# Kernel tuning notes

Measured on AMD Instinct MI355X. Metric: run time of the kernel, lower is better.

The kernel has to match this reference:

```python
import jax, jax.numpy as jnp
import numpy as np


def setup_inputs() -> dict:
    key = jax.random.key(0)
    ks = jax.random.split(key, 5)
    B, C, D, H, W = 2, 256, 8, 28, 28
    mid = C // 2
    # Kaiming-normal-ish init (std = sqrt(2/fan_in)) for 1x1 conv weights
    def kaiming(k, shape, fan_in):
        return jax.random.normal(k, shape, dtype=jnp.float32) * np.sqrt(2.0 / fan_in)
    x = jax.random.normal(ks[0], (B, C, D, H, W), dtype=jnp.float32)
    w1 = kaiming(ks[1], (mid, C), C)
    w2 = kaiming(ks[2], (mid, C), C)
    w3 = kaiming(ks[3], (mid, C), C)
    w4 = kaiming(ks[4], (C, mid), mid)
    b1 = jnp.zeros((mid,), jnp.float32)
    b2 = jnp.zeros((mid,), jnp.float32)
    b3 = jnp.zeros((mid,), jnp.float32)
    b4 = jnp.zeros((C,), jnp.float32)
    return {"x": x, "w1": w1, "b1": b1, "w2": w2, "b2": b2,
            "w3": w3, "b3": b3, "w4": w4, "b4": b4}


def reference(x, w1, b1, w2, b2, w3, b3, w4, b4):
    # x: [B, C, D, H, W]; 1x1x1 Conv3d == channel matmul over flattened N = D*H*W
    B, C, D, H, W = x.shape
    N = D * H * W
    xf = x.reshape(B, C, N)                                   # [B, C, N]
    # theta: conv1 -> [B, N, mid]
    e1 = jnp.einsum('mc,bcn->bnm', w1, xf) + b1               # [B, N, mid]
    # phi: conv2 -> [B, mid, N]
    e2 = jnp.einsum('mc,bcn->bmn', w2, xf) + b2[:, None]      # [B, mid, N]
    # g: conv3 -> [B, N, mid]
    e3 = jnp.einsum('mc,bcn->bnm', w3, xf) + b3               # [B, N, mid]
    # unscaled attention: softmax over keys (last axis)
    kernel = jnp.einsum('bnm,bmk->bnk', e1, e2)               # [B, N, N]
    kernel = jax.nn.softmax(kernel, axis=2)
    attn = jnp.einsum('bnk,bkm->bnm', kernel, e3)             # [B, N, mid]
    # conv4 (1x1 Conv1d): mid -> C, applied on [B, mid, N]
    y = jnp.einsum('cm,bnm->bcn', w4, attn) + b4[:, None]     # [B, C, N]
    return x + y.reshape(B, C, D, H, W)
```

## Files before the change

### kernel.cpp

```cpp
#include <hip/hip_runtime.h>


#define BB  2
#define CC  256
#define NN  6272
#define MID 128
#define KS  4
#define QB  128
#define NT  (NN / 64)
#define LOG2E 1.4426950408889634f

typedef _Float16 half2_t __attribute__((ext_vector_type(2)));
typedef _Float16 half4_t __attribute__((ext_vector_type(4)));
typedef _Float16 half8_t __attribute__((ext_vector_type(8)));
typedef float    floatx16 __attribute__((ext_vector_type(16)));
typedef int      i32x2 __attribute__((ext_vector_type(2)));
typedef unsigned u32x4 __attribute__((ext_vector_type(4)));

__device__ __forceinline__ void fma4(float4& a, const float4 v, const float s) {
    a.x += v.x * s; a.y += v.y * s; a.z += v.z * s; a.w += v.w * s;
}
__device__ __forceinline__ float dot4(const float4 a, const float4 b) {
    return a.x * b.x + a.y * b.y + a.z * b.z + a.w * b.w;
}
__device__ __forceinline__ unsigned pkrtz(float a, float b) {
    return __builtin_bit_cast(unsigned, __builtin_amdgcn_cvt_pkrtz(a, b));
}

__global__ __launch_bounds__(256, 2) void proj_kernel(
    const float* __restrict__ x,
    const float* __restrict__ w1, const float* __restrict__ bi1,
    const float* __restrict__ w2, const float* __restrict__ bi2,
    const float* __restrict__ w3, const float* __restrict__ bi3,
    _Float16* __restrict__ Qg, _Float16* __restrict__ Kg, _Float16* __restrict__ VtG)
{
    const int t  = threadIdx.x;
    const int n0 = blockIdx.x * 64;
    const int pj = blockIdx.y;
    const int b  = blockIdx.z;
    const float* w  = (pj == 0) ? w1 : (pj == 1) ? w2 : w3;
    const float* bi = (pj == 0) ? bi1 : (pj == 1) ? bi2 : bi3;
    const float qs  = (pj == 0) ? LOG2E : 1.0f;

    __shared__ float xs[CC * 68];
    {
        const float* xb = x + (size_t)b * CC * NN;
        for (int r = t; r < CC * 16; r += 256) {
            int c = r >> 4, j = (r & 15) << 2;
            float4 v = *(const float4*)(xb + (size_t)c * NN + n0 + j);
            *(float4*)&xs[c * 68 + j] = v;
        }
    }
    __syncthreads();

    const int n4 = (t & 15) << 2;
    const int m0 = (t >> 4) << 3;
    float4 acc4[8];
    #pragma unroll
    for (int k = 0; k < 8; ++k) acc4[k] = make_float4(0.f, 0.f, 0.f, 0.f);

    for (int cc = 0; cc < CC; cc += 4) {
        float4 xv[4];
        #pragma unroll
        for (int u = 0; u < 4; ++u)
            xv[u] = *(const float4*)&xs[(cc + u) * 68 + n4];
        #pragma unroll
        for (int k = 0; k < 8; ++k) {
            float4 wq = *(const float4*)(w + (size_t)(m0 + k) * CC + cc);
            fma4(acc4[k], xv[0], wq.x);
            fma4(acc4[k], xv[1], wq.y);
            fma4(acc4[k], xv[2], wq.z);
            fma4(acc4[k], xv[3], wq.w);
        }
    }

    const float* af = (const float*)acc4;
    float bb[8];
    #pragma unroll
    for (int k = 0; k < 8; ++k) bb[k] = bi[m0 + k];

    if (pj < 2) {
        _Float16* eo = ((pj == 0) ? Qg : Kg) + (size_t)b * NN * MID;
        #pragma unroll
        for (int i = 0; i < 4; ++i) {
            half8_t h;
            #pragma unroll
            for (int k = 0; k < 8; ++k) h[k] = (_Float16)((af[k * 4 + i] + bb[k]) * qs);
            *(half8_t*)(eo + (size_t)(n0 + n4 + i) * MID + m0) = h;
        }
    } else {
        _Float16* eo = VtG + (size_t)b * MID * NN;
        #pragma unroll
        for (int k = 0; k < 8; ++k) {
            half4_t h;
            #pragma unroll
            for (int i = 0; i < 4; ++i) h[i] = (_Float16)(af[k * 4 + i] + bb[k]);
            *(half4_t*)(eo + (size_t)(m0 + k) * NN + n0 + n4) = h;
        }
    }
}

__global__ __launch_bounds__(256, 2) void attn_kernel(
    const _Float16* __restrict__ Qg, const _Float16* __restrict__ Kg,
    const _Float16* __restrict__ VtG, _Float16* __restrict__ Opart,
    float* __restrict__ MLg)
{
    const int t    = threadIdx.x;
    const int lane = t & 63;
    const int wave = t >> 6;
    const int l31  = lane & 31;
    const int l5   = lane >> 5;
    const int q0   = blockIdx.x * QB;
    const int sp   = blockIdx.y;
    const int b    = blockIdx.z;
    const int kt0  = (NT * sp) / KS;
    const int kt1  = (NT * (sp + 1)) / KS;

    __shared__ __align__(16) char lds[52224];
    _Float16* Ks0 = (_Float16*)lds;
    _Float16* Ks1 = (_Float16*)(lds + 17408);
    _Float16* Vt  = (_Float16*)(lds + 34816);
    _Float16* Osh = (_Float16*)lds;

    const _Float16* Qb = Qg + ((size_t)b * NN + q0 + wave * 32) * MID;
    const _Float16* Kb = Kg + (size_t)b * NN * MID;
    const _Float16* Vb = VtG + (size_t)b * MID * NN;

    half8_t qf[8];
    #pragma unroll
    for (int ds = 0; ds < 8; ++ds)
        qf[ds] = *(const half8_t*)(Qb + (size_t)l31 * MID + ds * 16 + l5 * 8);

    floatx16 o[4];
    #pragma unroll
    for (int dt = 0; dt < 4; ++dt)
        #pragma unroll
        for (int j = 0; j < 16; ++j) o[dt][j] = 0.f;
    float m_run = -3.0e38f, l_run = 0.f;

    const int krow_t = t >> 4, koff_t = (t & 15) * 8;
    const int vd_t   = t >> 3, voff_t = (t & 7) * 8;

    #pragma unroll
    for (int it = 0; it < 4; ++it) {
        int r = it * 16 + krow_t;
        *(half8_t*)(Ks0 + r * 136 + koff_t) =
            *(const half8_t*)(Kb + (size_t)(kt0 * 64 + r) * MID + koff_t);
    }
    __syncthreads();

    for (int kt = kt0, cbuf = 0; kt < kt1; ++kt, cbuf ^= 1) {
        const int nk = kt * 64;
        _Float16* KBcur = cbuf ? Ks1 : Ks0;
        _Float16* KBnxt = cbuf ? Ks0 : Ks1;

        const int nk2 = (kt + 1 < kt1) ? nk + 64 : nk;
        half8_t vreg[4], kreg[4];
        #pragma unroll
        for (int it = 0; it < 4; ++it)
            vreg[it] = *(const half8_t*)(Vb + (size_t)(it * 32 + vd_t) * NN + nk + voff_t);
        #pragma unroll
        for (int it = 0; it < 4; ++it)
            kreg[it] = *(const half8_t*)(Kb + (size_t)(nk2 + it * 16 + krow_t) * MID + koff_t);
        __builtin_amdgcn_sched_barrier(0);

        floatx16 s0, s1;
        #pragma unroll
        for (int j = 0; j < 16; ++j) { s0[j] = 0.f; s1[j] = 0.f; }
        const _Float16* krow0 = KBcur + l31 * 136 + l5 * 8;
        const _Float16* krow1 = KBcur + (32 + l31) * 136 + l5 * 8;
        #pragma unroll
        for (int ds = 0; ds < 8; ++ds) {
            s0 = __builtin_amdgcn_mfma_f32_32x32x16_f16(
                     *(const half8_t*)(krow0 + ds * 16), qf[ds], s0, 0, 0, 0);
            s1 = __builtin_amdgcn_mfma_f32_32x32x16_f16(
                     *(const half8_t*)(krow1 + ds * 16), qf[ds], s1, 0, 0, 0);
        }

        float tmax = fmaxf(s0[0], s1[0]);
        #pragma unroll
        for (int j = 1; j < 16; ++j) tmax = fmaxf(tmax, fmaxf(s0[j], s1[j]));
        tmax = fmaxf(tmax, __shfl_xor(tmax, 32));

        if (!__all(tmax <= m_run)) {
            const float m_new = fmaxf(m_run, tmax);
            const float alpha = exp2f(m_run - m_new);
            m_run = m_new;
            l_run *= alpha;
            #pragma unroll
            for (int dt = 0; dt < 4; ++dt)
                #pragma unroll
                for (int j = 0; j < 16; ++j) o[dt][j] *= alpha;
        }

        float psum = 0.f;
        unsigned u0[8], u1[8];
        #pragma unroll
        for (int g = 0; g < 4; ++g) {
            float p0 = exp2f(s0[4 * g + 0] - m_run);
            float p1 = exp2f(s0[4 * g + 1] - m_run);
            float p2 = exp2f(s0[4 * g + 2] - m_run);
            float p3 = exp2f(s0[4 * g + 3] - m_run);
            psum += (p0 + p1) + (p2 + p3);
            u0[g] = pkrtz(p0, p1);
            u1[g] = pkrtz(p2, p3);
        }
        #pragma unroll
        for (int g = 0; g < 4; ++g) {
            float p0 = exp2f(s1[4 * g + 0] - m_run);
            float p1 = exp2f(s1[4 * g + 1] - m_run);
            float p2 = exp2f(s1[4 * g + 2] - m_run);
            float p3 = exp2f(s1[4 * g + 3] - m_run);
            psum += (p0 + p1) + (p2 + p3);
            u0[4 + g] = pkrtz(p0, p1);
            u1[4 + g] = pkrtz(p2, p3);
        }
        psum += __shfl_xor(psum, 32);
        l_run += psum;

        #pragma unroll
        for (int it = 0; it < 4; ++it)
            *(half8_t*)(Vt + (it * 32 + vd_t) * 68 + voff_t) = vreg[it];
        #pragma unroll
        for (int it = 0; it < 4; ++it)
            *(half8_t*)(KBnxt + (it * 16 + krow_t) * 136 + koff_t) = kreg[it];
        __syncthreads();

        #pragma unroll
        for (int ks = 0; ks < 4; ++ks) {
            i32x2 rA = __builtin_amdgcn_permlane32_swap(
                           (int)u0[2 * ks], (int)u0[2 * ks + 1], false, false);
            i32x2 rB = __builtin_amdgcn_permlane32_swap(
                           (int)u1[2 * ks], (int)u1[2 * ks + 1], false, false);
            u32x4 pw;
            pw[0] = (unsigned)rA[0]; pw[1] = (unsigned)rB[0];
            pw[2] = (unsigned)rA[1]; pw[3] = (unsigned)rB[1];
            half8_t pf = __builtin_bit_cast(half8_t, pw);
            const _Float16* vcol = Vt + ks * 16 + l5 * 8;
            #pragma unroll
            for (int dt = 0; dt < 4; ++dt)
                o[dt] = __builtin_amdgcn_mfma_f32_32x32x16_f16(
                            *(const half8_t*)(vcol + (dt * 32 + l31) * 68), pf,
                            o[dt], 0, 0, 0);
        }
        __syncthreads();
    }

    if (l5 == 0) {
        float* mlb = MLg + ((size_t)(b * KS + sp) * 2) * NN;
        mlb[q0 + wave * 32 + l31]      = m_run;
        mlb[NN + q0 + wave * 32 + l31] = l_run;
    }

    #pragma unroll
    for (int dt = 0; dt < 4; ++dt)
        #pragma unroll
        for (int h = 0; h < 4; ++h) {
            half4_t v;
            #pragma unroll
            for (int i = 0; i < 4; ++i) v[i] = (_Float16)o[dt][4 * h + i];
            *(half4_t*)(Osh + (wave * 32 + l31) * 136 + dt * 32 + 8 * h + 4 * l5) = v;
        }
    __syncthreads();
    _Float16* Ob = Opart + ((size_t)(b * KS + sp) * NN + q0) * MID;
    #pragma unroll
    for (int it = 0; it < 8; ++it) {
        int c = it * 256 + t;
        int q = c >> 4, g = c & 15;
        *(half8_t*)(Ob + (size_t)q * MID + g * 8) =
            *(const half8_t*)(Osh + q * 136 + g * 8);
    }
}

__global__ __launch_bounds__(256, 4) void comb_kernel(
    const _Float16* __restrict__ Opart, const float* __restrict__ MLg,
    _Float16* __restrict__ attnW)
{
    const int t  = threadIdx.x;
    const int b  = blockIdx.y;
    const int q  = blockIdx.x * 32 + (t >> 3);
    const int dg = (t & 7) * 16;

    float mv[KS], lv[KS];
    float m_g = -3.0e38f;
    #pragma unroll
    for (int s = 0; s < KS; ++s) {
        const float* mlb = MLg + ((size_t)(b * KS + s) * 2) * NN;
        mv[s] = mlb[q];
        lv[s] = mlb[NN + q];
        m_g = fmaxf(m_g, mv[s]);
    }
    float lg = 0.f, w[KS];
    #pragma unroll
    for (int s = 0; s < KS; ++s) { w[s] = exp2f(mv[s] - m_g); lg += lv[s] * w[s]; }
    const float inv = 1.0f / lg;

    float acc[16];
    #pragma unroll
    for (int j = 0; j < 16; ++j) acc[j] = 0.f;
    #pragma unroll
    for (int s = 0; s < KS; ++s) {
        const half8_t* Op = (const half8_t*)(Opart + ((size_t)(b * KS + s) * NN + q) * MID + dg);
        half8_t v0 = Op[0], v1 = Op[1];
        #pragma unroll
        for (int j = 0; j < 8; ++j) {
            acc[j]     += (float)v0[j] * w[s];
            acc[8 + j] += (float)v1[j] * w[s];
        }
    }
    half8_t h0, h1;
    #pragma unroll
    for (int j = 0; j < 8; ++j) {
        h0[j] = (_Float16)(acc[j] * inv);
        h1[j] = (_Float16)(acc[8 + j] * inv);
    }
    half8_t* Ow = (half8_t*)(attnW + ((size_t)b * NN + q) * MID + dg);
    Ow[0] = h0; Ow[1] = h1;
}

__global__ __launch_bounds__(256, 2) void epi_kernel(
    const _Float16* __restrict__ attnW, const float* __restrict__ w4,
    const float* __restrict__ b4, const float* __restrict__ x,
    float* __restrict__ out)
{
    const int t  = threadIdx.x;
    const int n0 = blockIdx.x * 64;
    const int b  = blockIdx.y;

    __shared__ float as[64 * 132];
    for (int r = t; r < 64 * 16; r += 256) {
        int q = r >> 4, g = r & 15;
        half8_t v = *(const half8_t*)(attnW + ((size_t)b * NN + n0 + q) * MID + g * 8);
        float* dst = &as[q * 132 + g * 8];
        #pragma unroll
        for (int j = 0; j < 8; ++j) dst[j] = (float)v[j];
    }
    __syncthreads();

    const int n4 = (t & 15) << 2;
    const int c0 = (t >> 4) << 4;
    float4 accE[16];
    #pragma unroll
    for (int k = 0; k < 16; ++k) accE[k] = make_float4(0.f, 0.f, 0.f, 0.f);

    for (int ms = 0; ms < 32; ++ms) {
        float4 av[4];
        #pragma unroll
        for (int i = 0; i < 4; ++i)
            av[i] = *(const float4*)&as[(n4 + i) * 132 + (ms << 2)];
        #pragma unroll
        for (int k = 0; k < 16; ++k) {
            float4 wq = *(const float4*)(w4 + (size_t)(c0 + k) * MID + (ms << 2));
            accE[k].x += dot4(av[0], wq);
            accE[k].y += dot4(av[1], wq);
            accE[k].z += dot4(av[2], wq);
            accE[k].w += dot4(av[3], wq);
        }
    }

    #pragma unroll
    for (int k = 0; k < 16; ++k) {
        const int c = c0 + k;
        const float bv = b4[c];
        const size_t off = ((size_t)b * CC + c) * NN + n0 + n4;
        float4 xr = *(const float4*)(x + off);
        float4 r;
        r.x = accE[k].x + bv + xr.x;
        r.y = accE[k].y + bv + xr.y;
        r.z = accE[k].z + bv + xr.z;
        r.w = accE[k].w + bv + xr.w;
        *(float4*)(out + off) = r;
    }
}

extern "C" void kernel_launch(void* const* d_in, const int* in_sizes, int n_in,
                              void* d_out, int out_size, void* d_ws, size_t ws_size,
                              hipStream_t stream)
{
    const float* x  = (const float*)d_in[0];
    const float* w1 = (const float*)d_in[1];
    const float* b1 = (const float*)d_in[2];
    const float* w2 = (const float*)d_in[3];
    const float* b2 = (const float*)d_in[4];
    const float* w3 = (const float*)d_in[5];
    const float* b3 = (const float*)d_in[6];
    const float* w4 = (const float*)d_in[7];
    const float* b4 = (const float*)d_in[8];
    float* out = (float*)d_out;

    _Float16* Qg    = (_Float16*)d_ws;
    _Float16* Kg    = Qg + (size_t)BB * NN * MID;
    _Float16* VtG   = Kg + (size_t)BB * NN * MID;
    _Float16* attnW = VtG + (size_t)BB * NN * MID;
    float* MLg      = (float*)(attnW + (size_t)BB * NN * MID);
    _Float16* Opart = (_Float16*)d_out;

    proj_kernel<<<dim3(NN / 64, 3, BB), 256, 0, stream>>>(x, w1, b1, w2, b2, w3, b3, Qg, Kg, VtG);
    attn_kernel<<<dim3(NN / QB, KS, BB), 256, 0, stream>>>(Qg, Kg, VtG, Opart, MLg);
    comb_kernel<<<dim3(NN / 32, BB), 256, 0, stream>>>(Opart, MLg, attnW);
    epi_kernel<<<dim3(NN / 64, BB), 256, 0, stream>>>(attnW, w4, b4, x, out);
}
```

Before: 302.7 us.

## Use fp16 MFMA with hi/lo split for projections and output conv

The fp32 scalar FMA loops in the QKV projection and output 1x1 conv kernels are replaced by 32x32x16 fp16 MFMA instructions. In the projection, x is split into fp16 hi and lo parts so accuracy stays near fp32 while running on matrix cores. One block now computes all three projections for a 64-column tile, so x is loaded once instead of three times. Weights are converted to fp16 on the fly, which loses some weight precision, and the output stores become strided scalar writes that may coalesce poorly.

```diff
diff --git a/kernel.cpp b/kernel.cpp
--- a/kernel.cpp
+++ b/kernel.cpp
@@ -17,14 +17,16 @@
 typedef int      i32x2 __attribute__((ext_vector_type(2)));
 typedef unsigned u32x4 __attribute__((ext_vector_type(4)));
 
-__device__ __forceinline__ void fma4(float4& a, const float4 v, const float s) {
-    a.x += v.x * s; a.y += v.y * s; a.z += v.z * s; a.w += v.w * s;
-}
-__device__ __forceinline__ float dot4(const float4 a, const float4 b) {
-    return a.x * b.x + a.y * b.y + a.z * b.z + a.w * b.w;
-}
 __device__ __forceinline__ unsigned pkrtz(float a, float b) {
     return __builtin_bit_cast(unsigned, __builtin_amdgcn_cvt_pkrtz(a, b));
+}
+__device__ __forceinline__ half8_t cvt8(const float* p) {
+    float4 f0 = *(const float4*)p;
+    float4 f1 = *(const float4*)(p + 4);
+    u32x4 u;
+    u[0] = pkrtz(f0.x, f0.y); u[1] = pkrtz(f0.z, f0.w);
+    u[2] = pkrtz(f1.x, f1.y); u[3] = pkrtz(f1.z, f1.w);
+    return __builtin_bit_cast(half8_t, u);
 }
 
 __global__ __launch_bounds__(256, 2) void proj_kernel(
@@ -34,68 +36,84 @@
     const float* __restrict__ w3, const float* __restrict__ bi3,
     _Float16* __restrict__ Qg, _Float16* __restrict__ Kg, _Float16* __restrict__ VtG)
 {
-    const int t  = threadIdx.x;
-    const int n0 = blockIdx.x * 64;
-    const int pj = blockIdx.y;
-    const int b  = blockIdx.z;
-    const float* w  = (pj == 0) ? w1 : (pj == 1) ? w2 : w3;
-    const float* bi = (pj == 0) ? bi1 : (pj == 1) ? bi2 : bi3;
-    const float qs  = (pj == 0) ? LOG2E : 1.0f;
-
-    __shared__ float xs[CC * 68];
-    {
-        const float* xb = x + (size_t)b * CC * NN;
-        for (int r = t; r < CC * 16; r += 256) {
-            int c = r >> 4, j = (r & 15) << 2;
-            float4 v = *(const float4*)(xb + (size_t)c * NN + n0 + j);
-            *(float4*)&xs[c * 68 + j] = v;
-        }
-    }
-    __syncthreads();
-
-    const int n4 = (t & 15) << 2;
-    const int m0 = (t >> 4) << 3;
-    float4 acc4[8];
-    #pragma unroll
-    for (int k = 0; k < 8; ++k) acc4[k] = make_float4(0.f, 0.f, 0.f, 0.f);
-
-    for (int cc = 0; cc < CC; cc += 4) {
-        float4 xv[4];
-        #pragma unroll
-        for (int u = 0; u < 4; ++u)
-            xv[u] = *(const float4*)&xs[(cc + u) * 68 + n4];
-        #pragma unroll
-        for (int k = 0; k < 8; ++k) {
-            float4 wq = *(const float4*)(w + (size_t)(m0 + k) * CC + cc);
-            fma4(acc4[k], xv[0], wq.x);
-            fma4(acc4[k], xv[1], wq.y);
-            fma4(acc4[k], xv[2], wq.z);
-            fma4(acc4[k], xv[3], wq.w);
-        }
-    }
-
-    const float* af = (const float*)acc4;
-    float bb[8];
-    #pragma unroll
-    for (int k = 0; k < 8; ++k) bb[k] = bi[m0 + k];
-
-    if (pj < 2) {
-        _Float16* eo = ((pj == 0) ? Qg : Kg) + (size_t)b * NN * MID;
-        #pragma unroll
-        for (int i = 0; i < 4; ++i) {
-            half8_t h;
-            #pragma unroll
-            for (int k = 0; k < 8; ++k) h[k] = (_Float16)((af[k * 4 + i] + bb[k]) * qs);
-            *(half8_t*)(eo + (size_t)(n0 + n4 + i) * MID + m0) = h;
-        }
-    } else {
-        _Float16* eo = VtG + (size_t)b * MID * NN;
-        #pragma unroll
-        for (int k = 0; k < 8; ++k) {
-            half4_t h;
-            #pragma unroll
-            for (int i = 0; i < 4; ++i) h[i] = (_Float16)(af[k * 4 + i] + bb[k]);
-            *(half4_t*)(eo + (size_t)(m0 + k) * NN + n0 + n4) = h;
+    const int t    = threadIdx.x;
+    const int lane = t & 63;
+    const int wave = t >> 6;
+    const int l31  = lane & 31;
+    const int l5   = lane >> 5;
+    const int n0   = blockIdx.x * 64;
+    const int b    = blockIdx.y;
+
+    __shared__ _Float16 xhi[64 * 140];
+    __shared__ _Float16 xlo[64 * 140];
+
+    floatx16 acc[6];
+    #pragma unroll
+    for (int i = 0; i < 6; ++i)
+        #pragma unroll
+        for (int j = 0; j < 16; ++j) acc[i][j] = 0.f;
+
+    for (int phase = 0; phase < 2; ++phase) {
+        const int cb = phase * 128;
+        if (phase) __syncthreads();
+        for (int it = 0; it < 8; ++it) {
+            int r = it * 256 + t;
+            int c = r >> 4, j4 = (r & 15) << 2;
+            float4 v = *(const float4*)(x + ((size_t)b * CC + cb + c) * NN + n0 + j4);
+            float vv[4] = {v.x, v.y, v.z, v.w};
+            #pragma unroll
+            for (int i = 0; i < 4; ++i) {
+                _Float16 h = (_Float16)vv[i];
+                xhi[(j4 + i) * 140 + c] = h;
+                xlo[(j4 + i) * 140 + c] = (_Float16)(vv[i] - (float)h);
+            }
+        }
+        __syncthreads();
+
+        #pragma unroll
+        for (int i = 0; i < 6; ++i) {
+            const int tau = wave * 6 + i;
+            const int pj = tau >> 3, mt = (tau >> 1) & 3, nt = tau & 1;
+            const float* w = (pj == 0) ? w1 : (pj == 1) ? w2 : w3;
+            const float* wrow = w + (size_t)(mt * 32 + l31) * CC + cb + l5 * 8;
+            const _Float16* xr_hi = xhi + (nt * 32 + l31) * 140 + l5 * 8;
+            const _Float16* xr_lo = xlo + (nt * 32 + l31) * 140 + l5 * 8;
+            #pragma unroll
+            for (int ds = 0; ds < 8; ++ds) {
+                half8_t wf = cvt8(wrow + ds * 16);
+                half8_t ah = *(const half8_t*)(xr_hi + ds * 16);
+                half8_t al = *(const half8_t*)(xr_lo + ds * 16);
+                if (pj < 2) {
+                    acc[i] = __builtin_amdgcn_mfma_f32_32x32x16_f16(ah, wf, acc[i], 0, 0, 0);
+                    acc[i] = __builtin_amdgcn_mfma_f32_32x32x16_f16(al, wf, acc[i], 0, 0, 0);
+                } else {
+                    acc[i] = __builtin_amdgcn_mfma_f32_32x32x16_f16(wf, ah, acc[i], 0, 0, 0);
+                    acc[i] = __builtin_amdgcn_mfma_f32_32x32x16_f16(wf, al, acc[i], 0, 0, 0);
+                }
+            }
+        }
+    }
+
+    #pragma unroll
+    for (int i = 0; i < 6; ++i) {
+        const int tau = wave * 6 + i;
+        const int pj = tau >> 3, mt = (tau >> 1) & 3, nt = tau & 1;
+        if (pj < 2) {
+            const float bm = ((pj == 0) ? bi1 : bi2)[mt * 32 + l31];
+            const float sc = (pj == 0) ? LOG2E : 1.0f;
+            _Float16* eo = ((pj == 0) ? Qg : Kg) + (size_t)b * NN * MID;
+            #pragma unroll
+            for (int j = 0; j < 16; ++j) {
+                int n = n0 + nt * 32 + (j & 3) + 8 * (j >> 2) + 4 * l5;
+                eo[(size_t)n * MID + mt * 32 + l31] = (_Float16)((acc[i][j] + bm) * sc);
+            }
+        } else {
+            _Float16* eo = VtG + (size_t)b * MID * NN;
+            #pragma unroll
+            for (int j = 0; j < 16; ++j) {
+                int m = mt * 32 + (j & 3) + 8 * (j >> 2) + 4 * l5;
+                eo[(size_t)m * NN + n0 + nt * 32 + l31] = (_Float16)(acc[i][j] + bi3[m]);
+            }
         }
     }
 }
@@ -323,53 +341,36 @@
     const float* __restrict__ b4, const float* __restrict__ x,
     float* __restrict__ out)
 {
-    const int t  = threadIdx.x;
-    const int n0 = blockIdx.x * 64;
-    const int b  = blockIdx.y;
-
-    __shared__ float as[64 * 132];
-    for (int r = t; r < 64 * 16; r += 256) {
-        int q = r >> 4, g = r & 15;
-        half8_t v = *(const half8_t*)(attnW + ((size_t)b * NN + n0 + q) * MID + g * 8);
-        float* dst = &as[q * 132 + g * 8];
-        #pragma unroll
-        for (int j = 0; j < 8; ++j) dst[j] = (float)v[j];
-    }
-    __syncthreads();
-
-    const int n4 = (t & 15) << 2;
-    const int c0 = (t >> 4) << 4;
-    float4 accE[16];
-    #pragma unroll
-    for (int k = 0; k < 16; ++k) accE[k] = make_float4(0.f, 0.f, 0.f, 0.f);
-
-    for (int ms = 0; ms < 32; ++ms) {
-        float4 av[4];
-        #pragma unroll
-        for (int i = 0; i < 4; ++i)
-            av[i] = *(const float4*)&as[(n4 + i) * 132 + (ms << 2)];
-        #pragma unroll
-        for (int k = 0; k < 16; ++k) {
-            float4 wq = *(const float4*)(w4 + (size_t)(c0 + k) * MID + (ms << 2));
-            accE[k].x += dot4(av[0], wq);
-            accE[k].y += dot4(av[1], wq);
-            accE[k].z += dot4(av[2], wq);
-            accE[k].w += dot4(av[3], wq);
-        }
-    }
-
-    #pragma unroll
-    for (int k = 0; k < 16; ++k) {
-        const int c = c0 + k;
-        const float bv = b4[c];
-        const size_t off = ((size_t)b * CC + c) * NN + n0 + n4;
-        float4 xr = *(const float4*)(x + off);
-        float4 r;
-        r.x = accE[k].x + bv + xr.x;
-        r.y = accE[k].y + bv + xr.y;
-        r.z = accE[k].z + bv + xr.z;
-        r.w = accE[k].w + bv + xr.w;
-        *(float4*)(out + off) = r;
+    const int t    = threadIdx.x;
+    const int lane = t & 63;
+    const int wave = t >> 6;
+    const int l31  = lane & 31;
+    const int l5   = lane >> 5;
+    const int n0   = blockIdx.x * 64;
+    const int b    = blockIdx.y;
+
+    #pragma unroll
+    for (int i = 0; i < 4; ++i) {
+        const int tau = wave * 4 + i;
+        const int ct = tau >> 1, nt = tau & 1;
+        floatx16 acc;
+        #pragma unroll
+        for (int j = 0; j < 16; ++j) acc[j] = 0.f;
+
+        const float* wrow = w4 + (size_t)(ct * 32 + l31) * MID + l5 * 8;
+        const _Float16* brow = attnW + ((size_t)b * NN + n0 + nt * 32 + l31) * MID + l5 * 8;
+        #pragma unroll
+        for (int ds = 0; ds < 8; ++ds) {
+            half8_t wf = cvt8(wrow + ds * 16);
+            half8_t bf = *(const half8_t*)(brow + ds * 16);
+            acc = __builtin_amdgcn_mfma_f32_32x32x16_f16(wf, bf, acc, 0, 0, 0);
+        }
+        #pragma unroll
+        for (int j = 0; j < 16; ++j) {
+            int c = ct * 32 + (j & 3) + 8 * (j >> 2) + 4 * l5;
+            size_t off = ((size_t)b * CC + c) * NN + n0 + nt * 32 + l31;
+            out[off] = acc[j] + b4[c] + x[off];
+        }
     }
 }
 
@@ -395,7 +396,7 @@
     float* MLg      = (float*)(attnW + (size_t)BB * NN * MID);
     _Float16* Opart = (_Float16*)d_out;
 
-    proj_kernel<<<dim3(NN / 64, 3, BB), 256, 0, stream>>>(x, w1, b1, w2, b2, w3, b3, Qg, Kg, VtG);
+    proj_kernel<<<dim3(NN / 64, BB), 256, 0, stream>>>(x, w1, b1, w2, b2, w3, b3, Qg, Kg, VtG);
     attn_kernel<<<dim3(NN / QB, KS, BB), 256, 0, stream>>>(Qg, Kg, VtG, Opart, MLg);
     comb_kernel<<<dim3(NN / 32, BB), 256, 0, stream>>>(Opart, MLg, attnW);
     epi_kernel<<<dim3(NN / 64, BB), 256, 0, stream>>>(attnW, w4, b4, x, out);
```

Measured after the change: 288.8 us. -4.6%, faster.
